# Performance work log

Measured on AMD Instinct MI355X. Metric: run time of the kernel, lower is better.

Reference implementation:

```python
import jax, jax.numpy as jnp
import numpy as np

N = 100000   # nodes
E = 800000   # edges
G = 64       # graphs in batch
H_LSTM = 256


def setup_inputs() -> dict:
    key = jax.random.key(0)
    ks = jax.random.split(key, 24)

    def rn(k, shape, scale=0.05):
        return jax.random.normal(k, shape, dtype=jnp.float32) * scale

    inp = {
        "x": jax.random.normal(ks[0], (N, 32), dtype=jnp.float32),
        "edge_index": jax.random.randint(ks[1], (2, E), 0, N, dtype=jnp.int64),
        "batch_idx": jnp.sort(jax.random.randint(ks[2], (N,), 0, G, dtype=jnp.int64)),
        # GCN layer weights (in_dim x out_dim) + bias
        "W1": rn(ks[3], (32, 128)),   "b1": jnp.zeros((128,), jnp.float32),
        "W2": rn(ks[4], (128, 256)),  "b2": jnp.zeros((256,), jnp.float32),
        "W3": rn(ks[5], (256, 512)),  "b3": jnp.zeros((512,), jnp.float32),
        # LSTM layer 0: input 512 -> hidden 256, gates order (i,f,g,o)
        "Wih0": rn(ks[6], (4 * H_LSTM, 512)), "Whh0": rn(ks[7], (4 * H_LSTM, H_LSTM)),
        "bih0": jnp.zeros((4 * H_LSTM,), jnp.float32), "bhh0": jnp.zeros((4 * H_LSTM,), jnp.float32),
        # LSTM layer 1: input 256 -> hidden 256
        "Wih1": rn(ks[8], (4 * H_LSTM, H_LSTM)), "Whh1": rn(ks[9], (4 * H_LSTM, H_LSTM)),
        "bih1": jnp.zeros((4 * H_LSTM,), jnp.float32), "bhh1": jnp.zeros((4 * H_LSTM,), jnp.float32),
        # output projection 256 -> 512
        "Wp": rn(ks[10], (512, H_LSTM)), "bp": jnp.zeros((512,), jnp.float32),
    }
    return inp


def _lstm_cell(xt, Wih, Whh, bih, bhh):
    B = xt.shape[0]
    H = Whh.shape[1]
    h0 = jnp.zeros((B, H), xt.dtype)
    c0 = jnp.zeros((B, H), xt.dtype)
    gates = xt @ Wih.T + h0 @ Whh.T + bih + bhh  # [B, 4H]
    i = jax.nn.sigmoid(gates[:, 0 * H:1 * H])
    f = jax.nn.sigmoid(gates[:, 1 * H:2 * H])
    g = jnp.tanh(gates[:, 2 * H:3 * H])
    o = jax.nn.sigmoid(gates[:, 3 * H:4 * H])
    c = f * c0 + i * g
    return o * jnp.tanh(c)


def reference(x, edge_index, batch_idx, W1, b1, W2, b2, W3, b3,
              Wih0, Whh0, bih0, bhh0, Wih1, Whh1, bih1, bhh1, Wp, bp):
    src, dst = edge_index[0], edge_index[1]
    # symmetric GCN normalization with self-loops (PyG GCNConv default)
    deg = jax.ops.segment_sum(jnp.ones((E,), x.dtype), dst, num_segments=N) + 1.0
    dinv = jax.lax.rsqrt(deg)
    edge_norm = (dinv[src] * dinv[dst])[:, None]
    self_norm = (dinv * dinv)[:, None]

    def gcn(h, W, b):
        h = h @ W                                            # transform first (smaller gather)
        msg = h[src] * edge_norm                             # [E, out]
        agg = jax.ops.segment_sum(msg, dst, num_segments=N)  # scatter-add to targets
        agg = agg + h * self_norm                            # self-loop contribution
        return jax.nn.relu(agg + b)

    h = gcn(x, W1, b1)
    h = gcn(h, W2, b2)
    h = gcn(h, W3, b3)  # [N, 512]

    # global mean pool per graph
    counts = jax.ops.segment_sum(jnp.ones((N,), h.dtype), batch_idx, num_segments=G)
    pooled = jax.ops.segment_sum(h, batch_idx, num_segments=G) / jnp.maximum(counts, 1.0)[:, None]

    # 2-layer LSTM over seq_len=1 (zero initial state)
    h1 = _lstm_cell(pooled, Wih0, Whh0, bih0, bhh0)
    h2 = _lstm_cell(h1, Wih1, Whh1, bih1, bhh1)
    return h2 @ Wp.T + bp  # [G, 512]
```

## Files before the change

### kernel.cpp

```cpp
#include <hip/hip_runtime.h>
#include <math.h>
#include <type_traits>


__device__ __forceinline__ float bf2f(unsigned short u) {
    union { unsigned int i; float f; } v; v.i = ((unsigned int)u) << 16; return v.f;
}
__device__ __forceinline__ unsigned short f2bf(float f) {
    union { float f_; unsigned int i; } v; v.f_ = f;
    unsigned int x = v.i;
    return (unsigned short)((x + 0x7fffu + ((x >> 16) & 1u)) >> 16);
}
__device__ __forceinline__ float sigm(float x) { return 1.f / (1.f + expf(-x)); }

typedef __attribute__((ext_vector_type(8))) short short8;
typedef __attribute__((ext_vector_type(16))) float f32x16;


__global__ void k_init(int* __restrict__ indeg, int* __restrict__ cursor,
                       int* __restrict__ gstart, int* __restrict__ gend,
                       float* __restrict__ pooled, int N) {
    int i = blockIdx.x * 256 + threadIdx.x;
    if (i < N) indeg[i] = 0;
    else if (i < 2 * N) cursor[i - N] = 0;
    else if (i < 2 * N + 64) gstart[i - 2 * N] = 0;
    else if (i < 2 * N + 128) gend[i - 2 * N - 64] = 0;
    else if (i < 2 * N + 128 + 64 * 512) pooled[i - 2 * N - 128] = 0.f;
}


template <int K, int NC>
__device__ __forceinline__ void prep_elem(const float* __restrict__ W,
                                          unsigned short* __restrict__ Wf, int idx) {
    constexpr int S = K / 16;
    int lane = idx & 63;
    int ts = idx >> 6;
    int s = ts % S, t = ts / S;
    int n = t * 32 + (lane & 31);
    int kb = s * 16 + (lane >> 5) * 8;
    short8 o;
    #pragma unroll
    for (int j = 0; j < 8; ++j) o[j] = (short)f2bf(W[(size_t)(kb + j) * NC + n]);
    *(short8*)(Wf + (size_t)idx * 8) = o;
}

__global__ void k_count(const int* __restrict__ dst, int* __restrict__ indeg, int E,
                        const float* __restrict__ W1, unsigned short* __restrict__ Wf1,
                        const float* __restrict__ W2, unsigned short* __restrict__ Wf2,
                        const float* __restrict__ W3, unsigned short* __restrict__ Wf3) {
    constexpr int P1 = 32 * 128 / 8, P2 = 128 * 256 / 8, P3 = 256 * 512 / 8;
    int i = blockIdx.x * 256 + threadIdx.x;
    if (i < E) atomicAdd(&indeg[dst[i]], 1);
    if (i < P1) prep_elem<32, 128>(W1, Wf1, i);
    else if (i < P1 + P2) prep_elem<128, 256>(W2, Wf2, i - P1);
    else if (i < P1 + P2 + P3) prep_elem<256, 512>(W3, Wf3, i - P1 - P2);
}


__global__ __launch_bounds__(1024) void k_scan1(const int* __restrict__ in, int* __restrict__ out,
                                                int* __restrict__ bsum, float* __restrict__ dinv,
                                                int N) {
    __shared__ int sd[1024];
    int tid = threadIdx.x;
    int i = blockIdx.x * 1024 + tid;
    int v = (i < N) ? in[i] : 0;
    if (i < N) dinv[i] = rsqrtf((float)v + 1.0f);
    sd[tid] = v;
    __syncthreads();
    for (int s = 1; s < 1024; s <<= 1) {
        int t = (tid >= s) ? sd[tid - s] : 0;
        __syncthreads();
        sd[tid] += t;
        __syncthreads();
    }
    if (i < N) out[i] = sd[tid] - v;
    if (tid == 1023) bsum[blockIdx.x] = sd[1023];
}

__global__ __launch_bounds__(256) void k_scan2(int* __restrict__ bsum, int nb) {
    __shared__ int sd[256];
    int tid = threadIdx.x;
    int v = (tid < nb) ? bsum[tid] : 0;
    sd[tid] = v;
    __syncthreads();
    for (int s = 1; s < 256; s <<= 1) {
        int t = (tid >= s) ? sd[tid - s] : 0;
        __syncthreads();
        sd[tid] += t;
        __syncthreads();
    }
    if (tid < nb) bsum[tid] = sd[tid] - v;
    if (tid == 0) bsum[nb] = sd[255];
}

__global__ __launch_bounds__(1024) void k_scan3(int* __restrict__ off, const int* __restrict__ bsum,
                                                const int* __restrict__ batch,
                                                int* __restrict__ gstart, int* __restrict__ gend,
                                                int N, int nb) {
    int i = blockIdx.x * 1024 + threadIdx.x;
    if (i < N) {
        off[i] += bsum[i >> 10];
        int g = batch[i];
        if (i == 0 || batch[i - 1] != g) gstart[g] = i;
        if (i == N - 1 || batch[i + 1] != g) gend[g] = i + 1;
    } else if (i == N) {
        off[N] = bsum[nb];
    }
}

__global__ void k_fill(const int* __restrict__ src, const int* __restrict__ dst,
                       const float* __restrict__ dinv, const int* __restrict__ off,
                       int* __restrict__ cursor, int* __restrict__ csrc,
                       float* __restrict__ cw, int E) {
    int i = blockIdx.x * 256 + threadIdx.x;
    if (i >= E) return;
    int d = dst[i], s = src[i];
    int p = off[d] + atomicAdd(&cursor[d], 1);
    csrc[p] = s;
    cw[p] = dinv[s] * dinv[d];
}


template <int F, typename T>
__device__ __forceinline__ void agg_body(
        const T* __restrict__ Hin, const float* __restrict__ dinv,
        const int* __restrict__ off, const int* __restrict__ csrc,
        const float* __restrict__ cw, unsigned short* __restrict__ out, int N) {
    constexpr int R = (F >= 256) ? 4 : (F >= 128 ? 2 : 1);
    int wave = (int)((blockIdx.x * 256u + threadIdx.x) >> 6);
    int lane = threadIdx.x & 63;
    if (wave >= N) return;
    int fb = (F >= 64) ? lane * R : lane;
    bool act = fb < F;
    int s0 = off[wave], s1 = off[wave + 1];
    float dn = dinv[wave], sn = dn * dn;
    float acc[R];
    #pragma unroll
    for (int j = 0; j < R; ++j) acc[j] = 0.f;
    if (act) {
        const T* ps = Hin + (size_t)wave * F + fb;
        if constexpr (std::is_same_v<T, float>) {
            acc[0] = ps[0] * sn;
        } else if constexpr (R == 4) {
            ushort4 hv = *(const ushort4*)ps;
            acc[0] = bf2f(hv.x) * sn; acc[1] = bf2f(hv.y) * sn;
            acc[2] = bf2f(hv.z) * sn; acc[3] = bf2f(hv.w) * sn;
        } else {
            ushort2 hv = *(const ushort2*)ps;
            acc[0] = bf2f(hv.x) * sn; acc[1] = bf2f(hv.y) * sn;
        }
    }
    int last = s1 - 1;
    for (int e = s0; e < s1; e += 8) {
        int   idx[8];
        float wgt[8];
        #pragma unroll
        for (int j = 0; j < 8; ++j) {
            int ee = e + j;
            int ec = ee <= last ? ee : last;
            idx[j] = csrc[ec];
            wgt[j] = (ee <= last) ? cw[ec] : 0.f;
        }
        if (act) {
            if constexpr (std::is_same_v<T, float>) {
                float d0[8];
                #pragma unroll
                for (int j = 0; j < 8; ++j) d0[j] = Hin[(size_t)idx[j] * F + fb];
                #pragma unroll
                for (int j = 0; j < 8; ++j) acc[0] += d0[j] * wgt[j];
            } else if constexpr (R == 4) {
                ushort4 d0[8];
                #pragma unroll
                for (int j = 0; j < 8; ++j)
                    d0[j] = *(const ushort4*)(Hin + (size_t)idx[j] * F + fb);
                #pragma unroll
                for (int j = 0; j < 8; ++j) {
                    float w = wgt[j];
                    acc[0] += bf2f(d0[j].x) * w; acc[1] += bf2f(d0[j].y) * w;
                    acc[2] += bf2f(d0[j].z) * w; acc[3] += bf2f(d0[j].w) * w;
                }
            } else {
                ushort2 d0[8];
                #pragma unroll
                for (int j = 0; j < 8; ++j)
                    d0[j] = *(const ushort2*)(Hin + (size_t)idx[j] * F + fb);
                #pragma unroll
                for (int j = 0; j < 8; ++j) {
                    float w = wgt[j];
                    acc[0] += bf2f(d0[j].x) * w; acc[1] += bf2f(d0[j].y) * w;
                }
            }
        }
    }
    if (act) {
        unsigned short* pd = out + (size_t)wave * F + fb;
        if constexpr (R == 4) {
            ushort4 o; o.x = f2bf(acc[0]); o.y = f2bf(acc[1]);
            o.z = f2bf(acc[2]); o.w = f2bf(acc[3]);
            *(ushort4*)pd = o;
        } else if constexpr (R == 2) {
            ushort2 o; o.x = f2bf(acc[0]); o.y = f2bf(acc[1]);
            *(ushort2*)pd = o;
        } else {
            pd[0] = f2bf(acc[0]);
        }
    }
}

__global__ __launch_bounds__(256) void k_aggL1(
        const float* __restrict__ Hin, const float* __restrict__ dinv,
        const int* __restrict__ off, const int* __restrict__ csrc,
        const float* __restrict__ cw, unsigned short* __restrict__ out, int N) {
    agg_body<32, float>(Hin, dinv, off, csrc, cw, out, N);
}

__global__ __launch_bounds__(256) void k_aggL2(
        const unsigned short* __restrict__ Hin, const float* __restrict__ dinv,
        const int* __restrict__ off, const int* __restrict__ csrc,
        const float* __restrict__ cw, unsigned short* __restrict__ out, int N) {
    agg_body<128, unsigned short>(Hin, dinv, off, csrc, cw, out, N);
}

__global__ __launch_bounds__(256) void k_aggL3pair(
        const unsigned short* __restrict__ Hin, const float* __restrict__ dinv,
        const int* __restrict__ off, const int* __restrict__ csrc,
        const float* __restrict__ cw, unsigned short* __restrict__ out, int N) {
    constexpr int F = 256;
    int wave = (int)((blockIdx.x * 256u + threadIdx.x) >> 6);
    int lane = threadIdx.x & 63;
    if (wave >= N) return;
    int half = lane >> 5;
    int fb = (lane & 31) * 8;
    int s0 = off[wave], s1 = off[wave + 1];
    int last = s1 - 1;
    float acc[8];
    #pragma unroll
    for (int k = 0; k < 8; ++k) acc[k] = 0.f;

    for (int e = s0; e < s1; e += 16) {
        int   idx[8];
        float wgt[8];
        #pragma unroll
        for (int j = 0; j < 8; ++j) {
            int ee = e + j * 2 + half;
            int ec = ee <= last ? ee : last;
            idx[j] = csrc[ec];
            wgt[j] = (ee <= last) ? cw[ec] : 0.f;
        }
        short8 d0[8];
        #pragma unroll
        for (int j = 0; j < 8; ++j)
            d0[j] = *(const short8*)(Hin + (size_t)idx[j] * F + fb);
        #pragma unroll
        for (int j = 0; j < 8; ++j) {
            float w = wgt[j];
            #pragma unroll
            for (int k = 0; k < 8; ++k)
                acc[k] += bf2f((unsigned short)d0[j][k]) * w;
        }
    }
    #pragma unroll
    for (int k = 0; k < 8; ++k) acc[k] += __shfl_xor(acc[k], 32, 64);

    if (half == 0) {
        float dn = dinv[wave], sn = dn * dn;
        short8 selfv = *(const short8*)(Hin + (size_t)wave * F + fb);
        short8 o;
        #pragma unroll
        for (int k = 0; k < 8; ++k)
            o[k] = (short)f2bf(acc[k] + bf2f((unsigned short)selfv[k]) * sn);
        *(short8*)(out + (size_t)wave * F + fb) = o;
    }
}


template <int K, int NC, int POOL>
__device__ __forceinline__ void gemm_body(
        const unsigned short* __restrict__ A, const unsigned short* __restrict__ Wf,
        const float* __restrict__ bias, unsigned short* __restrict__ C,
        float* __restrict__ pooled, float* __restrict__ partial,
        int* __restrict__ gtile, const int* __restrict__ batch, int M) {
    constexpr int S = K / 16;
    constexpr int CPR = K / 8;
    constexpr int NT = NC / 32;
    __shared__ unsigned short sA[64 * K];
    __shared__ int sbat[POOL ? 64 : 1];
    int tid = threadIdx.x, lane = tid & 63, w = tid >> 6;
    int q = lane >> 5, m = lane & 31;
    int row0 = blockIdx.x * 64;

    if (POOL) {
        if (tid < 64) { int rr = row0 + tid; if (rr > M - 1) rr = M - 1; sbat[tid] = batch[rr]; }
    }

    #pragma unroll
    for (int i = 0; i < (64 * CPR) / 256; ++i) {
        int g = i * 256 + tid;
        int mm = g / CPR, kc = g % CPR;
        int grow = row0 + mm; if (grow > M - 1) grow = M - 1;
        short8 v = *(const short8*)(A + (size_t)grow * K + kc * 8);
        int xm = (CPR >= 8) ? (mm & 7) : ((mm >> 1) & 3);
        *(short8*)(sA + (size_t)(mm * CPR + (kc ^ xm)) * 8) = v;
    }
    __syncthreads();

    int gmin = 0; bool fast = false;
    unsigned int selMask = 0;
    if (POOL) {
        gmin = sbat[0];
        fast = (sbat[63] - gmin) <= 1;
        if (tid == 0) gtile[blockIdx.x] = gmin;
        #pragma unroll
        for (int half = 0; half < 2; ++half) {
            #pragma unroll
            for (int j = 0; j < 16; ++j) {
                int rloc = half * 32 + (j & 3) + 8 * (j >> 2) + 4 * q;
                if (sbat[rloc] != gmin) selMask |= 1u << (half * 16 + j);
            }
        }
    }

    const short8* Wf8 = (const short8*)Wf;
    for (int t = w; t < NT; t += 4) {
        short8 bF[S];
        #pragma unroll
        for (int s = 0; s < S; ++s) bF[s] = Wf8[(t * S + s) * 64 + lane];
        int colBase = t * 32 + m;
        float bv = bias[colBase];
        float p0 = 0.f, p1 = 0.f;
        #pragma unroll
        for (int half = 0; half < 2; ++half) {
            int mrow = half * 32 + m;
            int xm = (CPR >= 8) ? (mrow & 7) : ((mrow >> 1) & 3);
            f32x16 acc;
            #pragma unroll
            for (int j = 0; j < 16; ++j) acc[j] = 0.f;
            #pragma unroll
            for (int s = 0; s < S; ++s) {
                int kc = s * 2 + q;
                short8 aF = *(const short8*)(sA + (size_t)(mrow * CPR + (kc ^ xm)) * 8);
                acc = __builtin_amdgcn_mfma_f32_32x32x16_bf16(aF, bF[s], acc, 0, 0, 0);
            }
            #pragma unroll
            for (int j = 0; j < 16; ++j) {
                int rloc = half * 32 + (j & 3) + 8 * (j >> 2) + 4 * q;
                int row = row0 + rloc;
                if (row < M) {
                    float v = fmaxf(acc[j] + bv, 0.f);
                    if (POOL) {
                        if (fast) {
                            bool sel = (selMask >> (half * 16 + j)) & 1u;
                            p0 += sel ? 0.f : v;
                            p1 += sel ? v : 0.f;
                        } else {
                            atomicAdd(&pooled[(size_t)sbat[rloc] * NC + colBase], v);
                        }
                    } else {
                        C[(size_t)row * NC + colBase] = f2bf(v);
                    }
                }
            }
        }
        if (POOL) {
            p0 += __shfl_xor(p0, 32, 64);
            p1 += __shfl_xor(p1, 32, 64);
            if (q == 0) {
                partial[((size_t)blockIdx.x * 2 + 0) * NC + colBase] = p0;
                partial[((size_t)blockIdx.x * 2 + 1) * NC + colBase] = p1;
            }
        }
    }
}

__global__ __launch_bounds__(256, 2) void k_gemmL1(
        const unsigned short* __restrict__ A, const unsigned short* __restrict__ Wf,
        const float* __restrict__ bias, unsigned short* __restrict__ C, int M) {
    gemm_body<32, 128, 0>(A, Wf, bias, C, nullptr, nullptr, nullptr, nullptr, M);
}

__global__ __launch_bounds__(256, 2) void k_gemmL2(
        const unsigned short* __restrict__ A, const unsigned short* __restrict__ Wf,
        const float* __restrict__ bias, unsigned short* __restrict__ C, int M) {
    gemm_body<128, 256, 0>(A, Wf, bias, C, nullptr, nullptr, nullptr, nullptr, M);
}

__global__ __launch_bounds__(256, 2) void k_gemmL3pool(
        const unsigned short* __restrict__ A, const unsigned short* __restrict__ Wf,
        const float* __restrict__ bias, float* __restrict__ pooled,
        float* __restrict__ partial, int* __restrict__ gtile,
        const int* __restrict__ batch, int M) {
    gemm_body<256, 512, 1>(A, Wf, bias, nullptr, pooled, partial, gtile, batch, M);
}


__global__ __launch_bounds__(256) void k_pool(
        const float* __restrict__ pooled, const float* __restrict__ partial,
        const int* __restrict__ gtile,
        const int* __restrict__ gstart, const int* __restrict__ gend,
        float* __restrict__ xmean) {
    int g = blockIdx.x, tid = threadIdx.x;
    int gs = gstart[g], ge = gend[g];
    float inv = 1.f / fmaxf((float)(ge - gs), 1.f);
    float a0 = pooled[g * 512 + tid];
    float a1 = pooled[g * 512 + 256 + tid];
    if (ge > gs) {
        int t0 = gs >> 6, t1 = (ge - 1) >> 6;
        for (int t = t0; t <= t1; ++t) {
            unsigned int slot = (unsigned int)(g - gtile[t]);
            if (slot < 2u) {
                const float* p = partial + ((size_t)t * 2 + slot) * 512;
                a0 += p[tid];
                a1 += p[tid + 256];
            }
        }
    }
    xmean[g * 512 + tid]       = a0 * inv;
    xmean[g * 512 + 256 + tid] = a1 * inv;
}

__device__ __forceinline__ float dot8(const float* __restrict__ w,
                                      float4 x0, float4 x1) {
    float4 a = *(const float4*)w, b = *(const float4*)(w + 4);
    return a.x * x0.x + a.y * x0.y + a.z * x0.z + a.w * x0.w +
           b.x * x1.x + b.y * x1.y + b.z * x1.z + b.w * x1.w;
}
__device__ __forceinline__ float dot4(const float* __restrict__ w, float4 x) {
    float4 a = *(const float4*)w;
    return a.x * x.x + a.y * x.y + a.z * x.z + a.w * x.w;
}

__global__ __launch_bounds__(256) void k_lstm0(
        const float* __restrict__ xmean, const float* __restrict__ Wih0,
        const float* __restrict__ bih0, const float* __restrict__ bhh0,
        float* __restrict__ h1) {
    int wid = (int)((blockIdx.x * 256u + threadIdx.x) >> 6);
    int lane = threadIdx.x & 63;
    int g = wid >> 8, hu = wid & 255;
    int k0 = lane * 8;
    const float* xp = xmean + g * 512 + k0;
    float4 x0 = *(const float4*)xp, x1 = *(const float4*)(xp + 4);
    float ai = dot8(Wih0 + (size_t)hu * 512 + k0, x0, x1);
    float ag = dot8(Wih0 + (size_t)(hu + 512) * 512 + k0, x0, x1);
    float ao = dot8(Wih0 + (size_t)(hu + 768) * 512 + k0, x0, x1);
    #pragma unroll
    for (int msk = 32; msk >= 1; msk >>= 1) {
        ai += __shfl_xor(ai, msk, 64);
        ag += __shfl_xor(ag, msk, 64);
        ao += __shfl_xor(ao, msk, 64);
    }
    if (lane == 0) {
        ai += bih0[hu]       + bhh0[hu];
        ag += bih0[hu + 512] + bhh0[hu + 512];
        ao += bih0[hu + 768] + bhh0[hu + 768];
        float c0 = sigm(ai) * tanhf(ag);
        h1[g * 256 + hu] = sigm(ao) * tanhf(c0);
    }
}

__global__ __launch_bounds__(256) void k_lstm1(
        const float* __restrict__ h1, const float* __restrict__ Wih1,
        const float* __restrict__ bih1, const float* __restrict__ bhh1,
        float* __restrict__ h2) {
    int wid = (int)((blockIdx.x * 256u + threadIdx.x) >> 6);
    int lane = threadIdx.x & 63;
    int g = wid >> 8, hu = wid & 255;
    int k0 = lane * 4;
    float4 x = *(const float4*)(h1 + g * 256 + k0);
    float ai = dot4(Wih1 + (size_t)hu * 256 + k0, x);
    float ag = dot4(Wih1 + (size_t)(hu + 512) * 256 + k0, x);
    float ao = dot4(Wih1 + (size_t)(hu + 768) * 256 + k0, x);
    #pragma unroll
    for (int msk = 32; msk >= 1; msk >>= 1) {
        ai += __shfl_xor(ai, msk, 64);
        ag += __shfl_xor(ag, msk, 64);
        ao += __shfl_xor(ao, msk, 64);
    }
    if (lane == 0) {
        ai += bih1[hu]       + bhh1[hu];
        ag += bih1[hu + 512] + bhh1[hu + 512];
        ao += bih1[hu + 768] + bhh1[hu + 768];
        float c1 = sigm(ai) * tanhf(ag);
        h2[g * 256 + hu] = sigm(ao) * tanhf(c1);
    }
}

__global__ __launch_bounds__(256) void k_out(
        const float* __restrict__ h2, const float* __restrict__ Wp,
        const float* __restrict__ bp, float* __restrict__ out) {
    int wid = (int)((blockIdx.x * 256u + threadIdx.x) >> 6);
    int lane = threadIdx.x & 63;
    int g = wid >> 9, r = wid & 511;
    int k0 = lane * 4;
    float4 x = *(const float4*)(h2 + g * 256 + k0);
    float a = dot4(Wp + (size_t)r * 256 + k0, x);
    #pragma unroll
    for (int msk = 32; msk >= 1; msk >>= 1) a += __shfl_xor(a, msk, 64);
    if (lane == 0) out[g * 512 + r] = a + bp[r];
}


extern "C" void kernel_launch(void* const* d_in, const int* in_sizes, int n_in,
                              void* d_out, int out_size, void* d_ws, size_t ws_size,
                              hipStream_t stream) {
    const float* x     = (const float*)d_in[0];
    const int*   eidx  = (const int*)d_in[1];
    const int*   batch = (const int*)d_in[2];
    const float* W1 = (const float*)d_in[3];  const float* b1 = (const float*)d_in[4];
    const float* W2 = (const float*)d_in[5];  const float* b2 = (const float*)d_in[6];
    const float* W3 = (const float*)d_in[7];  const float* b3 = (const float*)d_in[8];
    const float* Wih0 = (const float*)d_in[9];
    const float* bih0 = (const float*)d_in[11];
    const float* bhh0 = (const float*)d_in[12];
    const float* Wih1 = (const float*)d_in[13];
    const float* bih1 = (const float*)d_in[15];
    const float* bhh1 = (const float*)d_in[16];
    const float* Wp = (const float*)d_in[17]; const float* bp = (const float*)d_in[18];
    float* out = (float*)d_out;

    const int N = in_sizes[0] / 32;
    const int E = in_sizes[1] / 2;
    const int* src = eidx;
    const int* dst = eidx + E;
    const int rowTiles = (N + 63) / 64;

    char* w = (char*)d_ws;
    auto alloc = [&](size_t bytes) {
        char* p = w;
        w += (bytes + 255) & ~(size_t)255;
        return p;
    };
    unsigned short* buf1 = (unsigned short*)alloc((size_t)N * 256 * 2);
    unsigned short* buf2 = (unsigned short*)alloc((size_t)N * 256 * 2);
    unsigned short* Wf1  = (unsigned short*)alloc(128 * 32 * 2);
    unsigned short* Wf2  = (unsigned short*)alloc(256 * 128 * 2);
    unsigned short* Wf3  = (unsigned short*)alloc(512 * 256 * 2);
    int*   indeg  = (int*)alloc((size_t)N * 4);
    int*   off    = (int*)alloc((size_t)(N + 1) * 4);
    int*   cursor = (int*)alloc((size_t)N * 4);
    float* dinv   = (float*)alloc((size_t)N * 4);
    int*   csrc   = (int*)alloc((size_t)E * 4);
    float* cw     = (float*)alloc((size_t)E * 4);
    int*   bsum   = (int*)alloc(8192);
    int*   gstart = (int*)alloc(64 * 4);
    int*   gend   = (int*)alloc(64 * 4);
    float* pooled = (float*)alloc(64 * 512 * 4);
    float* xmean  = (float*)alloc(64 * 512 * 4);
    float* h1buf  = (float*)alloc(64 * 256 * 4);
    float* h2buf  = (float*)alloc(64 * 256 * 4);

    float* partial = (float*)csrc;
    int*   gtile   = cursor;

    int initTot = 2 * N + 128 + 64 * 512;
    k_init<<<(initTot + 255) / 256, 256, 0, stream>>>(indeg, cursor, gstart, gend, pooled, N);
    k_count<<<(E + 255) / 256, 256, 0, stream>>>(dst, indeg, E, W1, Wf1, W2, Wf2, W3, Wf3);
    int nb = (N + 1023) / 1024;
    k_scan1<<<nb, 1024, 0, stream>>>(indeg, off, bsum, dinv, N);
    k_scan2<<<1, 256, 0, stream>>>(bsum, nb);
    k_scan3<<<(N + 1 + 1023) / 1024, 1024, 0, stream>>>(off, bsum, batch, gstart, gend, N, nb);
    k_fill<<<(E + 255) / 256, 256, 0, stream>>>(src, dst, dinv, off, cursor, csrc, cw, E);

    int aggBlocks = (N + 3) / 4;

    k_aggL1<<<aggBlocks, 256, 0, stream>>>(x, dinv, off, csrc, cw, buf1, N);
    k_gemmL1<<<rowTiles, 256, 0, stream>>>(buf1, Wf1, b1, buf2, N);
    k_aggL2<<<aggBlocks, 256, 0, stream>>>(buf2, dinv, off, csrc, cw, buf1, N);
    k_gemmL2<<<rowTiles, 256, 0, stream>>>(buf1, Wf2, b2, buf2, N);
    k_aggL3pair<<<aggBlocks, 256, 0, stream>>>(buf2, dinv, off, csrc, cw, buf1, N);
    k_gemmL3pool<<<rowTiles, 256, 0, stream>>>(buf1, Wf3, b3, pooled, partial, gtile, batch, N);

    k_pool<<<64, 256, 0, stream>>>(pooled, partial, gtile, gstart, gend, xmean);
    k_lstm0<<<4096, 256, 0, stream>>>(xmean, Wih0, bih0, bhh0, h1buf);
    k_lstm1<<<4096, 256, 0, stream>>>(h1buf, Wih1, bih1, bhh1, h2buf);
    k_out<<<8192, 256, 0, stream>>>(h2buf, Wp, bp, out);
}
```

Measured before the change: 457.9 us.

## Factor GCN edge weights into per-node dinv scaling, drop per-edge weight array

Instead of storing a per-edge weight dinv[s]*dinv[d] and multiplying each gathered neighbour row by it, the source-side dinv is folded into the producer (pre-scaled x in the scan kernel, and the GEMM epilogues for layers 1-2), and the destination-side dinv is applied once after the unweighted sum. Padding lanes now gather the node's own row, and a count correction subtracts those extra self contributions while adding the self-loop term. This removes the cw array, its writes in k_fill and its reads in every aggregation, at the cost of an extra pre-scaled copy of x and a small float correction trick that changes rounding slightly. csrc is padded by 64 entries to allow unguarded over-reads.

After: 457.5 us. No clear change (-0.1%).

```diff
diff --git a/kernel.cpp b/kernel.cpp
--- a/kernel.cpp
+++ b/kernel.cpp
@@ -59,12 +59,16 @@
 
 __global__ __launch_bounds__(1024) void k_scan1(const int* __restrict__ in, int* __restrict__ out,
                                                 int* __restrict__ bsum, float* __restrict__ dinv,
+                                                const float* __restrict__ x, float* __restrict__ xs,
                                                 int N) {
     __shared__ int sd[1024];
+    __shared__ float sdv[1024];
     int tid = threadIdx.x;
     int i = blockIdx.x * 1024 + tid;
     int v = (i < N) ? in[i] : 0;
-    if (i < N) dinv[i] = rsqrtf((float)v + 1.0f);
+    float dv = rsqrtf((float)v + 1.0f);
+    if (i < N) dinv[i] = dv;
+    sdv[tid] = dv;
     sd[tid] = v;
     __syncthreads();
     for (int s = 1; s < 1024; s <<= 1) {
@@ -75,6 +79,20 @@
     }
     if (i < N) out[i] = sd[tid] - v;
     if (tid == 1023) bsum[blockIdx.x] = sd[1023];
+    int base = blockIdx.x * 1024;
+    const float4* x4 = (const float4*)x;
+    float4* xs4 = (float4*)xs;
+    #pragma unroll
+    for (int rep = 0; rep < 8; ++rep) {
+        int j = rep * 1024 + tid;
+        int node = base + (j >> 3);
+        if (node < N) {
+            float4 t = x4[(size_t)base * 8 + j];
+            float s = sdv[j >> 3];
+            t.x *= s; t.y *= s; t.z *= s; t.w *= s;
+            xs4[(size_t)base * 8 + j] = t;
+        }
+    }
 }
 
 __global__ __launch_bounds__(256) void k_scan2(int* __restrict__ bsum, int nb) {
@@ -109,15 +127,13 @@
 }
 
 __global__ void k_fill(const int* __restrict__ src, const int* __restrict__ dst,
-                       const float* __restrict__ dinv, const int* __restrict__ off,
-                       int* __restrict__ cursor, int* __restrict__ csrc,
-                       float* __restrict__ cw, int E) {
+                       const int* __restrict__ off, int* __restrict__ cursor,
+                       int* __restrict__ csrc, int E) {
     int i = blockIdx.x * 256 + threadIdx.x;
     if (i >= E) return;
-    int d = dst[i], s = src[i];
+    int d = dst[i];
     int p = off[d] + atomicAdd(&cursor[d], 1);
-    csrc[p] = s;
-    cw[p] = dinv[s] * dinv[d];
+    csrc[p] = src[i];
 }
 
 
@@ -125,7 +141,7 @@
 __device__ __forceinline__ void agg_body(
         const T* __restrict__ Hin, const float* __restrict__ dinv,
         const int* __restrict__ off, const int* __restrict__ csrc,
-        const float* __restrict__ cw, unsigned short* __restrict__ out, int N) {
+        unsigned short* __restrict__ out, int N) {
     constexpr int R = (F >= 256) ? 4 : (F >= 128 ? 2 : 1);
     int wave = (int)((blockIdx.x * 256u + threadIdx.x) >> 6);
     int lane = threadIdx.x & 63;
@@ -133,33 +149,20 @@
     int fb = (F >= 64) ? lane * R : lane;
     bool act = fb < F;
     int s0 = off[wave], s1 = off[wave + 1];
-    float dn = dinv[wave], sn = dn * dn;
+    int L = s1 - s0;
+    float corr = 1.0f - (float)(((L + 7) & ~7) - L);
+    float dn = dinv[wave];
     float acc[R];
     #pragma unroll
     for (int j = 0; j < R; ++j) acc[j] = 0.f;
-    if (act) {
-        const T* ps = Hin + (size_t)wave * F + fb;
-        if constexpr (std::is_same_v<T, float>) {
-            acc[0] = ps[0] * sn;
-        } else if constexpr (R == 4) {
-            ushort4 hv = *(const ushort4*)ps;
-            acc[0] = bf2f(hv.x) * sn; acc[1] = bf2f(hv.y) * sn;
-            acc[2] = bf2f(hv.z) * sn; acc[3] = bf2f(hv.w) * sn;
-        } else {
-            ushort2 hv = *(const ushort2*)ps;
-            acc[0] = bf2f(hv.x) * sn; acc[1] = bf2f(hv.y) * sn;
-        }
-    }
-    int last = s1 - 1;
+
     for (int e = s0; e < s1; e += 8) {
-        int   idx[8];
-        float wgt[8];
+        int idx[8];
         #pragma unroll
         for (int j = 0; j < 8; ++j) {
             int ee = e + j;
-            int ec = ee <= last ? ee : last;
-            idx[j] = csrc[ec];
-            wgt[j] = (ee <= last) ? cw[ec] : 0.f;
+            int ix = csrc[ee];
+            idx[j] = (ee < s1) ? ix : wave;
         }
         if (act) {
             if constexpr (std::is_same_v<T, float>) {
@@ -167,7 +170,7 @@
                 #pragma unroll
                 for (int j = 0; j < 8; ++j) d0[j] = Hin[(size_t)idx[j] * F + fb];
                 #pragma unroll
-                for (int j = 0; j < 8; ++j) acc[0] += d0[j] * wgt[j];
+                for (int j = 0; j < 8; ++j) acc[0] += d0[j];
             } else if constexpr (R == 4) {
                 ushort4 d0[8];
                 #pragma unroll
@@ -175,9 +178,8 @@
                     d0[j] = *(const ushort4*)(Hin + (size_t)idx[j] * F + fb);
                 #pragma unroll
                 for (int j = 0; j < 8; ++j) {
-                    float w = wgt[j];
-                    acc[0] += bf2f(d0[j].x) * w; acc[1] += bf2f(d0[j].y) * w;
-                    acc[2] += bf2f(d0[j].z) * w; acc[3] += bf2f(d0[j].w) * w;
+                    acc[0] += bf2f(d0[j].x); acc[1] += bf2f(d0[j].y);
+                    acc[2] += bf2f(d0[j].z); acc[3] += bf2f(d0[j].w);
                 }
             } else {
                 ushort2 d0[8];
@@ -186,23 +188,30 @@
                     d0[j] = *(const ushort2*)(Hin + (size_t)idx[j] * F + fb);
                 #pragma unroll
                 for (int j = 0; j < 8; ++j) {
-                    float w = wgt[j];
-                    acc[0] += bf2f(d0[j].x) * w; acc[1] += bf2f(d0[j].y) * w;
+                    acc[0] += bf2f(d0[j].x); acc[1] += bf2f(d0[j].y);
                 }
             }
         }
     }
     if (act) {
+        const T* ps = Hin + (size_t)wave * F + fb;
         unsigned short* pd = out + (size_t)wave * F + fb;
-        if constexpr (R == 4) {
-            ushort4 o; o.x = f2bf(acc[0]); o.y = f2bf(acc[1]);
-            o.z = f2bf(acc[2]); o.w = f2bf(acc[3]);
+        if constexpr (std::is_same_v<T, float>) {
+            pd[0] = f2bf((acc[0] + corr * ps[0]) * dn);
+        } else if constexpr (R == 4) {
+            ushort4 hv = *(const ushort4*)ps;
+            ushort4 o;
+            o.x = f2bf((acc[0] + corr * bf2f(hv.x)) * dn);
+            o.y = f2bf((acc[1] + corr * bf2f(hv.y)) * dn);
+            o.z = f2bf((acc[2] + corr * bf2f(hv.z)) * dn);
+            o.w = f2bf((acc[3] + corr * bf2f(hv.w)) * dn);
             *(ushort4*)pd = o;
-        } else if constexpr (R == 2) {
-            ushort2 o; o.x = f2bf(acc[0]); o.y = f2bf(acc[1]);
+        } else {
+            ushort2 hv = *(const ushort2*)ps;
+            ushort2 o;
+            o.x = f2bf((acc[0] + corr * bf2f(hv.x)) * dn);
+            o.y = f2bf((acc[1] + corr * bf2f(hv.y)) * dn);
             *(ushort2*)pd = o;
-        } else {
-            pd[0] = f2bf(acc[0]);
         }
     }
 }
@@ -210,21 +219,21 @@
 __global__ __launch_bounds__(256) void k_aggL1(
         const float* __restrict__ Hin, const float* __restrict__ dinv,
         const int* __restrict__ off, const int* __restrict__ csrc,
-        const float* __restrict__ cw, unsigned short* __restrict__ out, int N) {
-    agg_body<32, float>(Hin, dinv, off, csrc, cw, out, N);
+        unsigned short* __restrict__ out, int N) {
+    agg_body<32, float>(Hin, dinv, off, csrc, out, N);
 }
 
 __global__ __launch_bounds__(256) void k_aggL2(
         const unsigned short* __restrict__ Hin, const float* __restrict__ dinv,
         const int* __restrict__ off, const int* __restrict__ csrc,
-        const float* __restrict__ cw, unsigned short* __restrict__ out, int N) {
-    agg_body<128, unsigned short>(Hin, dinv, off, csrc, cw, out, N);
+        unsigned short* __restrict__ out, int N) {
+    agg_body<128, unsigned short>(Hin, dinv, off, csrc, out, N);
 }
 
 __global__ __launch_bounds__(256) void k_aggL3pair(
         const unsigned short* __restrict__ Hin, const float* __restrict__ dinv,
         const int* __restrict__ off, const int* __restrict__ csrc,
-        const float* __restrict__ cw, unsigned short* __restrict__ out, int N) {
+        unsigned short* __restrict__ out, int N) {
     constexpr int F = 256;
     int wave = (int)((blockIdx.x * 256u + threadIdx.x) >> 6);
     int lane = threadIdx.x & 63;
@@ -232,20 +241,19 @@
     int half = lane >> 5;
     int fb = (lane & 31) * 8;
     int s0 = off[wave], s1 = off[wave + 1];
-    int last = s1 - 1;
+    int L = s1 - s0;
+    float corrTot = 1.0f - (float)(((L + 15) & ~15) - L);
     float acc[8];
     #pragma unroll
     for (int k = 0; k < 8; ++k) acc[k] = 0.f;
 
     for (int e = s0; e < s1; e += 16) {
-        int   idx[8];
-        float wgt[8];
+        int idx[8];
         #pragma unroll
         for (int j = 0; j < 8; ++j) {
             int ee = e + j * 2 + half;
-            int ec = ee <= last ? ee : last;
-            idx[j] = csrc[ec];
-            wgt[j] = (ee <= last) ? cw[ec] : 0.f;
+            int ix = csrc[ee];
+            idx[j] = (ee < s1) ? ix : wave;
         }
         short8 d0[8];
         #pragma unroll
@@ -253,22 +261,21 @@
             d0[j] = *(const short8*)(Hin + (size_t)idx[j] * F + fb);
         #pragma unroll
         for (int j = 0; j < 8; ++j) {
-            float w = wgt[j];
             #pragma unroll
             for (int k = 0; k < 8; ++k)
-                acc[k] += bf2f((unsigned short)d0[j][k]) * w;
+                acc[k] += bf2f((unsigned short)d0[j][k]);
         }
     }
     #pragma unroll
     for (int k = 0; k < 8; ++k) acc[k] += __shfl_xor(acc[k], 32, 64);
 
     if (half == 0) {
-        float dn = dinv[wave], sn = dn * dn;
+        float dn = dinv[wave];
         short8 selfv = *(const short8*)(Hin + (size_t)wave * F + fb);
         short8 o;
         #pragma unroll
         for (int k = 0; k < 8; ++k)
-            o[k] = (short)f2bf(acc[k] + bf2f((unsigned short)selfv[k]) * sn);
+            o[k] = (short)f2bf((acc[k] + corrTot * bf2f((unsigned short)selfv[k])) * dn);
         *(short8*)(out + (size_t)wave * F + fb) = o;
     }
 }
@@ -277,7 +284,8 @@
 template <int K, int NC, int POOL>
 __device__ __forceinline__ void gemm_body(
         const unsigned short* __restrict__ A, const unsigned short* __restrict__ Wf,
-        const float* __restrict__ bias, unsigned short* __restrict__ C,
+        const float* __restrict__ bias, const float* __restrict__ dinv,
+        unsigned short* __restrict__ C,
         float* __restrict__ pooled, float* __restrict__ partial,
         int* __restrict__ gtile, const int* __restrict__ batch, int M) {
     constexpr int S = K / 16;
@@ -285,12 +293,15 @@
     constexpr int NT = NC / 32;
     __shared__ unsigned short sA[64 * K];
     __shared__ int sbat[POOL ? 64 : 1];
+    __shared__ float sdv[POOL ? 1 : 64];
     int tid = threadIdx.x, lane = tid & 63, w = tid >> 6;
     int q = lane >> 5, m = lane & 31;
     int row0 = blockIdx.x * 64;
 
-    if (POOL) {
-        if (tid < 64) { int rr = row0 + tid; if (rr > M - 1) rr = M - 1; sbat[tid] = batch[rr]; }
+    if (tid < 64) {
+        int rr = row0 + tid; if (rr > M - 1) rr = M - 1;
+        if (POOL) sbat[tid] = batch[rr];
+        else      sdv[tid] = dinv[rr];
     }
 
     #pragma unroll
@@ -356,7 +367,7 @@
                             atomicAdd(&pooled[(size_t)sbat[rloc] * NC + colBase], v);
                         }
                     } else {
-                        C[(size_t)row * NC + colBase] = f2bf(v);
+                        C[(size_t)row * NC + colBase] = f2bf(v * sdv[rloc]);
                     }
                 }
             }
@@ -374,14 +385,16 @@
 
 __global__ __launch_bounds__(256, 2) void k_gemmL1(
         const unsigned short* __restrict__ A, const unsigned short* __restrict__ Wf,
-        const float* __restrict__ bias, unsigned short* __restrict__ C, int M) {
-    gemm_body<32, 128, 0>(A, Wf, bias, C, nullptr, nullptr, nullptr, nullptr, M);
+        const float* __restrict__ bias, const float* __restrict__ dinv,
+        unsigned short* __restrict__ C, int M) {
+    gemm_body<32, 128, 0>(A, Wf, bias, dinv, C, nullptr, nullptr, nullptr, nullptr, M);
 }
 
 __global__ __launch_bounds__(256, 2) void k_gemmL2(
         const unsigned short* __restrict__ A, const unsigned short* __restrict__ Wf,
-        const float* __restrict__ bias, unsigned short* __restrict__ C, int M) {
-    gemm_body<128, 256, 0>(A, Wf, bias, C, nullptr, nullptr, nullptr, nullptr, M);
+        const float* __restrict__ bias, const float* __restrict__ dinv,
+        unsigned short* __restrict__ C, int M) {
+    gemm_body<128, 256, 0>(A, Wf, bias, dinv, C, nullptr, nullptr, nullptr, nullptr, M);
 }
 
 __global__ __launch_bounds__(256, 2) void k_gemmL3pool(
@@ -389,7 +402,7 @@
         const float* __restrict__ bias, float* __restrict__ pooled,
         float* __restrict__ partial, int* __restrict__ gtile,
         const int* __restrict__ batch, int M) {
-    gemm_body<256, 512, 1>(A, Wf, bias, nullptr, pooled, partial, gtile, batch, M);
+    gemm_body<256, 512, 1>(A, Wf, bias, nullptr, nullptr, pooled, partial, gtile, batch, M);
 }
 
 
@@ -538,8 +551,8 @@
     int*   off    = (int*)alloc((size_t)(N + 1) * 4);
     int*   cursor = (int*)alloc((size_t)N * 4);
     float* dinv   = (float*)alloc((size_t)N * 4);
-    int*   csrc   = (int*)alloc((size_t)E * 4);
-    float* cw     = (float*)alloc((size_t)E * 4);
+    int*   csrc   = (int*)alloc((size_t)(E + 64) * 4);
+    float* xs     = (float*)alloc((size_t)N * 32 * 4);
     int*   bsum   = (int*)alloc(8192);
     int*   gstart = (int*)alloc(64 * 4);
     int*   gend   = (int*)alloc(64 * 4);
@@ -548,25 +561,25 @@
     float* h1buf  = (float*)alloc(64 * 256 * 4);
     float* h2buf  = (float*)alloc(64 * 256 * 4);
 
-    float* partial = (float*)csrc;
+    float* partial = xs;
     int*   gtile   = cursor;
 
     int initTot = 2 * N + 128 + 64 * 512;
     k_init<<<(initTot + 255) / 256, 256, 0, stream>>>(indeg, cursor, gstart, gend, pooled, N);
     k_count<<<(E + 255) / 256, 256, 0, stream>>>(dst, indeg, E, W1, Wf1, W2, Wf2, W3, Wf3);
     int nb = (N + 1023) / 1024;
-    k_scan1<<<nb, 1024, 0, stream>>>(indeg, off, bsum, dinv, N);
+    k_scan1<<<nb, 1024, 0, stream>>>(indeg, off, bsum, dinv, x, xs, N);
     k_scan2<<<1, 256, 0, stream>>>(bsum, nb);
     k_scan3<<<(N + 1 + 1023) / 1024, 1024, 0, stream>>>(off, bsum, batch, gstart, gend, N, nb);
-    k_fill<<<(E + 255) / 256, 256, 0, stream>>>(src, dst, dinv, off, cursor, csrc, cw, E);
+    k_fill<<<(E + 255) / 256, 256, 0, stream>>>(src, dst, off, cursor, csrc, E);
 
     int aggBlocks = (N + 3) / 4;
 
-    k_aggL1<<<aggBlocks, 256, 0, stream>>>(x, dinv, off, csrc, cw, buf1, N);
-    k_gemmL1<<<rowTiles, 256, 0, stream>>>(buf1, Wf1, b1, buf2, N);
-    k_aggL2<<<aggBlocks, 256, 0, stream>>>(buf2, dinv, off, csrc, cw, buf1, N);
-    k_gemmL2<<<rowTiles, 256, 0, stream>>>(buf1, Wf2, b2, buf2, N);
-    k_aggL3pair<<<aggBlocks, 256, 0, stream>>>(buf2, dinv, off, csrc, cw, buf1, N);
+    k_aggL1<<<aggBlocks, 256, 0, stream>>>(xs, dinv, off, csrc, buf1, N);
+    k_gemmL1<<<rowTiles, 256, 0, stream>>>(buf1, Wf1, b1, dinv, buf2, N);
+    k_aggL2<<<aggBlocks, 256, 0, stream>>>(buf2, dinv, off, csrc, buf1, N);
+    k_gemmL2<<<rowTiles, 256, 0, stream>>>(buf1, Wf2, b2, dinv, buf2, N);
+    k_aggL3pair<<<aggBlocks, 256, 0, stream>>>(buf2, dinv, off, csrc, buf1, N);
     k_gemmL3pool<<<rowTiles, 256, 0, stream>>>(buf1, Wf3, b3, pooled, partial, gtile, batch, N);
 
     k_pool<<<64, 256, 0, stream>>>(pooled, partial, gtile, gstart, gend, xmean);
```
